# Performance work log

Hardware: AMD Instinct MI355X
Metric: run time of the kernel (lower is better)

Reference implementation:

```python
import jax, jax.numpy as jnp
import numpy as np

N = 20000      # nodes per type
E = 320000     # edges per relation
F = 512        # raw feature dim
H = 4          # attention heads
C = 128        # hidden_channels per head
B = 64         # batch_size (num graphs)
HH = H * C
INNER = 64
NEG_SLOPE = 0.2


def _gatv2(x_src, x_dst, ei, Wl, Wr, att, b):
    """PyG GATv2Conv (concat=True, add_self_loops=True, neg_slope=0.2).
    x_src:[Ns,Fin] x_dst:[Nd,Fin'] ei:[2,E] Wl,Wr:[Fin,H*C] att:[H,C] b:[H*C].
    Returns [Nd, H*C]. Self-loop edges appended (inputs assumed loop-free)."""
    n_dst = x_dst.shape[0]
    loop = jnp.arange(min(x_src.shape[0], n_dst), dtype=ei.dtype)
    src = jnp.concatenate([ei[0], loop])
    dst = jnp.concatenate([ei[1], loop])
    xl = (x_src @ Wl).reshape(-1, H, C)   # source-side transform
    xr = (x_dst @ Wr).reshape(-1, H, C)   # target-side transform
    e = jax.nn.leaky_relu(xl[src] + xr[dst], NEG_SLOPE)   # [E',H,C]
    logit = jnp.einsum('ehc,hc->eh', e, att)               # [E',H]
    m = jax.ops.segment_max(logit, dst, num_segments=n_dst)
    m = jnp.where(jnp.isfinite(m), m, 0.0)
    p = jnp.exp(logit - m[dst])
    s = jax.ops.segment_sum(p, dst, num_segments=n_dst)
    alpha = p / jnp.maximum(s[dst], 1e-16)                 # per-dst softmax
    out = jax.ops.segment_sum(alpha[:, :, None] * xl[src], dst, num_segments=n_dst)
    return out.reshape(n_dst, HH) + b


def _layer(x_i, x_j, ei_ii, ei_jj, ei_ij, ei_ji, Wl, Wr, att, b):
    # relation order: 0:(x_i->x_i) 1:(x_j->x_j) 2:(x_i->x_j) 3:(x_j->x_i); HeteroConv aggr='sum'
    oi = _gatv2(x_i, x_i, ei_ii, Wl[0], Wr[0], att[0], b[0]) \
       + _gatv2(x_j, x_i, ei_ji, Wl[3], Wr[3], att[3], b[3])
    oj = _gatv2(x_j, x_j, ei_jj, Wl[1], Wr[1], att[1], b[1]) \
       + _gatv2(x_i, x_j, ei_ij, Wl[2], Wr[2], att[2], b[2])
    # head-sum + tanh: x.view(-1, heads, hidden).sum(1).tanh()
    oi = jnp.tanh(oi.reshape(-1, H, C).sum(axis=1))
    oj = jnp.tanh(oj.reshape(-1, H, C).sum(axis=1))
    return oi, oj


def setup_inputs() -> dict:
    key = jax.random.key(0)
    ks = jax.random.split(key, 24)
    inp = {
        'x_i': jax.random.normal(ks[0], (N, F), jnp.float32),
        'x_j': jax.random.normal(ks[1], (N, F), jnp.float32),
        'ei_ii': jax.random.randint(ks[2], (2, E), 0, N, jnp.int32),
        'ei_jj': jax.random.randint(ks[3], (2, E), 0, N, jnp.int32),
        'ei_ij': jax.random.randint(ks[4], (2, E), 0, N, jnp.int32),
        'ei_ji': jax.random.randint(ks[5], (2, E), 0, N, jnp.int32),
        'batch_i': jnp.sort(jax.random.randint(ks[6], (N,), 0, B, jnp.int32)),
        'batch_j': jnp.sort(jax.random.randint(ks[7], (N,), 0, B, jnp.int32)),
        'Wl0': jax.random.normal(ks[8], (4, F, HH), jnp.float32) / np.sqrt(F),
        'Wr0': jax.random.normal(ks[9], (4, F, HH), jnp.float32) / np.sqrt(F),
        'att0': jax.random.normal(ks[10], (4, H, C), jnp.float32) / np.sqrt(C),
        'b0': jnp.zeros((4, HH), jnp.float32),
        'Wl1': jax.random.normal(ks[11], (4, C, HH), jnp.float32) / np.sqrt(C),
        'Wr1': jax.random.normal(ks[12], (4, C, HH), jnp.float32) / np.sqrt(C),
        'att1': jax.random.normal(ks[13], (4, H, C), jnp.float32) / np.sqrt(C),
        'b1': jnp.zeros((4, HH), jnp.float32),
        'W_out': jax.random.normal(ks[14], (C, 1), jnp.float32) / np.sqrt(C),
        'b_out': jnp.zeros((1,), jnp.float32),
        'W_i': jax.random.normal(ks[15], (C, INNER), jnp.float32) / np.sqrt(C),
        'b_i': jnp.zeros((INNER,), jnp.float32),
        'W_j': jax.random.normal(ks[16], (C, INNER), jnp.float32) / np.sqrt(C),
        'b_j': jnp.zeros((INNER,), jnp.float32),
    }
    return inp


def reference(x_i, x_j, ei_ii, ei_jj, ei_ij, ei_ji, batch_i, batch_j,
              Wl0, Wr0, att0, b0, Wl1, Wr1, att1, b1,
              W_out, b_out, W_i, b_i, W_j, b_j):
    x_i, x_j = _layer(x_i, x_j, ei_ii, ei_jj, ei_ij, ei_ji, Wl0, Wr0, att0, b0)
    x_i, x_j = _layer(x_i, x_j, ei_ii, ei_jj, ei_ij, ei_ji, Wl1, Wr1, att1, b1)
    # global_add_pool per graph, then unsqueeze(1) + tanh
    p_i = jnp.tanh(jax.ops.segment_sum(x_i, batch_i, num_segments=B))[:, None, :]  # [B,1,C]
    p_j = jnp.tanh(jax.ops.segment_sum(x_j, batch_j, num_segments=B))[:, None, :]
    y_i = p_i @ W_i + b_i   # [B,1,INNER]
    y_j = p_j @ W_j + b_j
    x = (p_i + p_j)[:, 0, :]            # cat along dim=1 then sum(dim=1)
    logits = jax.nn.sigmoid(x @ W_out + b_out)   # [B,1]
    return (logits, y_i, y_j)
```

## Files before the change

### kernel.cpp

```cpp
#include <hip/hip_runtime.h>

#define NN      20000
#define EE      320000
#define ETOT    340000
#define FD      512
#define HH_     4
#define CD      128
#define HHD     512
#define BG      64
#define INNERD  64

typedef __attribute__((ext_vector_type(8))) short bf16x8;
typedef __attribute__((ext_vector_type(4))) float f32x4;

__device__ __forceinline__ float bf2f(unsigned v) { return __uint_as_float(v << 16); }
__device__ __forceinline__ unsigned short f2bf(float f) {
    unsigned u = __float_as_uint(f);
    unsigned r = 0x7fffu + ((u >> 16) & 1u);
    return (unsigned short)((u + r) >> 16);
}
__device__ __forceinline__ void load8bf(const unsigned short* p, float* f) {
    uint4 u = *reinterpret_cast<const uint4*>(p);
    f[0] = bf2f(u.x & 0xffffu); f[1] = bf2f(u.x >> 16);
    f[2] = bf2f(u.y & 0xffffu); f[3] = bf2f(u.y >> 16);
// ... 156 lines not shown
    const unsigned short* __restrict__ Blg, unsigned short* __restrict__ C,
    int bx, int by, int M, int K, int N)
{
    __shared__ unsigned short Ah[128][40];
    __shared__ unsigned short Al[A_EXACT ? 1 : 128][40];

    const int tid = threadIdx.x;
    const int wave = tid >> 6, lane = tid & 63;
    const int quad = lane >> 4, lrow = lane & 15;
    const int wr = (wave >> 1) * 64, wc = (wave & 1) * 64;
    const int tileM = by * 128, tileN = bx * 128;

    const int srow = tid >> 1;
    const int sks  = (tid & 1) * 16;
    const int sgm  = tileM + srow;

    const size_t bfrag = ((size_t)(tileN + wc + lrow) << 5) + quad * 8;
    const size_t kblk  = (size_t)N << 5;

    f32x4 acc[4][4] = {};

    for (int k0 = 0; k0 < K; k0 += 32) {
        if constexpr (!A_EXACT) {
            bf16x8 ph[2] = {{}, {}}, pl[2] = {{}, {}};
            if (sgm < M) {
                const float* Ap = (const float*)A + (size_t)sgm * K + k0 + sks;
                #pragma unroll
                for (int s = 0; s < 2; ++s) {
                    float4 f0 = reinterpret_cast<const float4*>(Ap)[2 * s];
                    float4 f1 = reinterpret_cast<const float4*>(Ap)[2 * s + 1];
                    float xv[8] = {f0.x, f0.y, f0.z, f0.w, f1.x, f1.y, f1.z, f1.w};
                    #pragma unroll
                    for (int pp = 0; pp < 4; ++pp) {
                        unsigned u0 = __float_as_uint(xv[2 * pp]);
                        unsigned u1 = __float_as_uint(xv[2 * pp + 1]);
                        reinterpret_cast<unsigned*>(&ph[s])[pp] =
                            __builtin_amdgcn_perm(u1, u0, 0x07060302u);
                        float r0 = xv[2 * pp]     - __uint_as_float(u0 & 0xffff0000u);
                        float r1 = xv[2 * pp + 1] - __uint_as_float(u1 & 0xffff0000u);
                        reinterpret_cast<unsigned*>(&pl[s])[pp] =
                            __builtin_amdgcn_perm(__float_as_uint(r1), __float_as_uint(r0), 0x07060302u);
                    }
                }
            }
            *reinterpret_cast<bf16x8*>(&Ah[srow][sks])     = ph[0];
            *reinterpret_cast<bf16x8*>(&Ah[srow][sks + 8]) = ph[1];
            *reinterpret_cast<bf16x8*>(&Al[srow][sks])     = pl[0];
            *reinterpret_cast<bf16x8*>(&Al[srow][sks + 8]) = pl[1];
        } else {
            bf16x8 v0 = {}, v1 = {};
            if (sgm < M) {
                const unsigned short* Ap = (const unsigned short*)A + (size_t)sgm * K + k0 + sks;
                v0 = reinterpret_cast<const bf16x8*>(Ap)[0];
                v1 = reinterpret_cast<const bf16x8*>(Ap)[1];
            }
            *reinterpret_cast<bf16x8*>(&Ah[srow][sks])     = v0;
            *reinterpret_cast<bf16x8*>(&Ah[srow][sks + 8]) = v1;
        }
        bf16x8 bh[4], bl[4];
        {
            const unsigned short* Bb = Bhg + (size_t)(k0 >> 5) * kblk + bfrag;
            const unsigned short* Bc = Blg + (size_t)(k0 >> 5) * kblk + bfrag;
            #pragma unroll
            for (int ni = 0; ni < 4; ++ni) {
                bh[ni] = *reinterpret_cast<const bf16x8*>(Bb + ((size_t)ni << 9));
                bl[ni] = *reinterpret_cast<const bf16x8*>(Bc + ((size_t)ni << 9));
            }
        }
        __syncthreads();
        bf16x8 ah[4], al[4];
        #pragma unroll
        for (int mi = 0; mi < 4; ++mi) {
            ah[mi] = *reinterpret_cast<const bf16x8*>(&Ah[wr + mi * 16 + lrow][quad * 8]);
            if constexpr (!A_EXACT)
                al[mi] = *reinterpret_cast<const bf16x8*>(&Al[wr + mi * 16 + lrow][quad * 8]);
        }
        #pragma unroll
        for (int mi = 0; mi < 4; ++mi)
            #pragma unroll
            for (int ni = 0; ni < 4; ++ni) {
                acc[mi][ni] = __builtin_amdgcn_mfma_f32_16x16x32_bf16(
                    ah[mi], bh[ni], acc[mi][ni], 0, 0, 0);
                acc[mi][ni] = __builtin_amdgcn_mfma_f32_16x16x32_bf16(
                    ah[mi], bl[ni], acc[mi][ni], 0, 0, 0);
                if constexpr (!A_EXACT)
                    acc[mi][ni] = __builtin_amdgcn_mfma_f32_16x16x32_bf16(
                        al[mi], bh[ni], acc[mi][ni], 0, 0, 0);
            }
        __syncthreads();
    }
    #pragma unroll
    for (int mi = 0; mi < 4; ++mi) {
        #pragma unroll
        for (int ni = 0; ni < 4; ++ni) {
            int gcol = tileN + wc + ni * 16 + lrow;
            #pragma unroll
            for (int r = 0; r < 4; ++r) {
                int grow = tileM + wr + mi * 16 + quad * 4 + r;
                if (grow < M)
                    C[(size_t)grow * N + gcol] = f2bf(acc[mi][ni][r]);
            }
        }
    }
}

template <typename TA, bool A_EXACT>
__global__ __launch_bounds__(256, 3) void gemm_mfma_t(
    const TA* __restrict__ A0, const TA* __restrict__ A1,
    const unsigned short* __restrict__ B0h, const unsigned short* __restrict__ B0l,
    const unsigned short* __restrict__ B1h, const unsigned short* __restrict__ B1l,
    unsigned short* __restrict__ C0, unsigned short* __restrict__ C1,
    int M, int K, int N)
{
    const int gx = gridDim.x, gy = gridDim.y;
    const int nwg = gx * gy * (int)gridDim.z;
    int b = ((int)blockIdx.z * gy + blockIdx.y) * gx + blockIdx.x;
    int xcd = b & 7, q8 = nwg >> 3, r8 = nwg & 7;
    int work = (xcd < r8 ? xcd * (q8 + 1) : r8 * (q8 + 1) + (xcd - r8) * q8) + (b >> 3);
    int bx = work % gx; int t2 = work / gx; int by = t2 % gy; int bz = t2 / gy;

    const TA* A = bz ? A1 : A0;
    const unsigned short* Bhg = bz ? B1h : B0h;
    const unsigned short* Blg = bz ? B1l : B0l;
    unsigned short* C = bz ? C1 : C0;
    gemm_body<TA, A_EXACT>(A, Bhg, Blg, C, bx, by, M, K, N);
}

template <typename TA, bool A_EXACT>
__global__ __launch_bounds__(256, 3) void gemm_mfma_t4(
    const TA* __restrict__ A0, const TA* __restrict__ A1,
    const TA* __restrict__ A2, const TA* __restrict__ A3,
    const unsigned short* __restrict__ B0h, const unsigned short* __restrict__ B0l,
    const unsigned short* __restrict__ B1h, const unsigned short* __restrict__ B1l,
    const unsigned short* __restrict__ B2h, const unsigned short* __restrict__ B2l,
    const unsigned short* __restrict__ B3h, const unsigned short* __restrict__ B3l,
    unsigned short* __restrict__ C0, unsigned short* __restrict__ C1,
    unsigned short* __restrict__ C2, unsigned short* __restrict__ C3,
    int M, int K, int N)
{
    const int gx = gridDim.x, gy = gridDim.y;
    const int nwg = gx * gy * (int)gridDim.z;
    int b = ((int)blockIdx.z * gy + blockIdx.y) * gx + blockIdx.x;
    int xcd = b & 7, q8 = nwg >> 3, r8 = nwg & 7;
    int work = (xcd < r8 ? xcd * (q8 + 1) : r8 * (q8 + 1) + (xcd - r8) * q8) + (b >> 3);
    int bx = work % gx; int t2 = work / gx; int by = t2 % gy; int bz = t2 / gy;

    const TA* A = bz == 0 ? A0 : bz == 1 ? A1 : bz == 2 ? A2 : A3;
    const unsigned short* Bhg = bz == 0 ? B0h : bz == 1 ? B1h : bz == 2 ? B2h : B3h;
    const unsigned short* Blg = bz == 0 ? B0l : bz == 1 ? B1l : bz == 2 ? B2l : B3l;
    unsigned short* C = bz == 0 ? C0 : bz == 1 ? C1 : bz == 2 ? C2 : C3;
    gemm_body<TA, A_EXACT>(A, Bhg, Blg, C, bx, by, M, K, N);
}

template <typename TA, bool A_EXACT>
__global__ __launch_bounds__(256) void gemm_mfma(
    const TA* __restrict__ A0, const TA* __restrict__ A1,
    const float* __restrict__ B0, const float* __restrict__ B1, int ldb,
    unsigned short* __restrict__ C0, unsigned short* __restrict__ C1,
    int M, int K, int N)
{
    const TA* A = blockIdx.z ? A1 : A0;
    const float* B = blockIdx.z ? B1 : B0;
    unsigned short* C = blockIdx.z ? C1 : C0;

    __shared__ unsigned short Ah[64][40];
    __shared__ unsigned short Al[64][40];
    __shared__ unsigned short Bh[64][40];
    __shared__ unsigned short Bl[64][40];
    const int tid = threadIdx.x;
    const int wave = tid >> 6, lane = tid & 63;
    const int quad = lane >> 4, lrow = lane & 15;
    const int tileM = blockIdx.y * 64, tileN = blockIdx.x * 64;
    const int wm = (wave >> 1) * 32, wn = (wave & 1) * 32;

    f32x4 acc[2][2] = {};

    const int am = tid >> 2;
    const int aks = (tid & 3) * 8;
    const int bn = tid & 63;
    const int bk0 = (tid >> 6) * 8;

    for (int k0 = 0; k0 < K; k0 += 32) {
        {
            int gm = tileM + am;
            bf16x8 ph = {}, pl = {};
            if (gm < M) {
                #pragma unroll
                for (int j = 0; j < 8; ++j) {
                    unsigned short h, l;
                    splitA(A, (size_t)gm * K + k0 + aks + j, h, l);
                    ph[j] = (short)h; pl[j] = (short)l;
                }
            }
            *reinterpret_cast<bf16x8*>(&Ah[am][aks]) = ph;
            if (!A_EXACT) *reinterpret_cast<bf16x8*>(&Al[am][aks]) = pl;
        }
        {
            bf16x8 ph, pl;
            #pragma unroll
            for (int j = 0; j < 8; ++j) {
                unsigned short h, l;
                split_f32(B[(size_t)(k0 + bk0 + j) * ldb + tileN + bn], h, l);
                ph[j] = (short)h; pl[j] = (short)l;
            }
            *reinterpret_cast<bf16x8*>(&Bh[bn][bk0]) = ph;
            *reinterpret_cast<bf16x8*>(&Bl[bn][bk0]) = pl;
        }
        __syncthreads();
        bf16x8 ah[2], al[2], bh[2], bl[2];
        #pragma unroll
        for (int mi = 0; mi < 2; ++mi) {
            ah[mi] = *reinterpret_cast<const bf16x8*>(&Ah[wm + mi * 16 + lrow][quad * 8]);
            if (!A_EXACT)
                al[mi] = *reinterpret_cast<const bf16x8*>(&Al[wm + mi * 16 + lrow][quad * 8]);
        }
        #pragma unroll
        for (int ni = 0; ni < 2; ++ni) {
            bh[ni] = *reinterpret_cast<const bf16x8*>(&Bh[wn + ni * 16 + lrow][quad * 8]);
            bl[ni] = *reinterpret_cast<const bf16x8*>(&Bl[wn + ni * 16 + lrow][quad * 8]);
        }
        #pragma unroll
        for (int mi = 0; mi < 2; ++mi)
            #pragma unroll
            for (int ni = 0; ni < 2; ++ni) {
                acc[mi][ni] = __builtin_amdgcn_mfma_f32_16x16x32_bf16(
                    ah[mi], bh[ni], acc[mi][ni], 0, 0, 0);
                acc[mi][ni] = __builtin_amdgcn_mfma_f32_16x16x32_bf16(
                    ah[mi], bl[ni], acc[mi][ni], 0, 0, 0);
                if (!A_EXACT)
                    acc[mi][ni] = __builtin_amdgcn_mfma_f32_16x16x32_bf16(
                        al[mi], bh[ni], acc[mi][ni], 0, 0, 0);
            }
        __syncthreads();
    }
    #pragma unroll
    for (int mi = 0; mi < 2; ++mi) {
        #pragma unroll
        for (int ni = 0; ni < 2; ++ni) {
            int gcol = tileN + wn + ni * 16 + lrow;
            #pragma unroll
            for (int r = 0; r < 4; ++r) {
                int grow = tileM + wm + mi * 16 + quad * 4 + r;
                if (grow < M)
                    C[(size_t)grow * N + gcol] = f2bf(acc[mi][ni][r]);
            }
        }
    }
}

__global__ __launch_bounds__(256) void fused_aggr1(
    const int* __restrict__ rowptr, const unsigned short* __restrict__ srcs,
    const unsigned short* __restrict__ xl, const unsigned short* __restrict__ xr,
    const float* __restrict__ att,
    float* __restrict__ acc, int add_in, int fin_mode,
    const float* __restrict__ bA, const float* __restrict__ bB,
    unsigned short* __restrict__ z,
    const int* __restrict__ batch, float* __restrict__ pool)
{
    int dst = (int)((blockIdx.x * (size_t)blockDim.x + threadIdx.x) >> 6);
    int lane = threadIdx.x & 63;
    if (dst >= NN) return;
    int beg = rowptr[dst], end = rowptr[dst + 1];

    unsigned ub = *reinterpret_cast<const unsigned*>(xr + (size_t)dst * CD + lane * 2);
    float br0 = bf2f(ub & 0xffffu), br1 = bf2f(ub >> 16);
    float ta0 = att[lane * 2], ta1 = att[lane * 2 + 1];

    float n0 = 0.f, n1 = 0.f, den = 0.f;
    for (int k = beg; k < end; ++k) {
        int src = srcs[k];
        unsigned ua = *reinterpret_cast<const unsigned*>(xl + (size_t)src * CD + lane * 2);
        float a0 = bf2f(ua & 0xffffu), a1 = bf2f(ua >> 16);
        float v0 = a0 + br0, v1 = a1 + br1;
        v0 = (v0 > 0.f) ? v0 : 0.2f * v0;
        v1 = (v1 > 0.f) ? v1 : 0.2f * v1;
        float d = v0 * ta0 + v1 * ta1;
        #pragma unroll
        for (int off = 1; off < 64; off <<= 1)
            d += __shfl_xor(d, off);
        float p = expf(d);
        n0 += p * a0; n1 += p * a1; den += p;
    }
    float o0 = n0 / den, o1 = n1 / den;
    size_t ai = (size_t)dst * CD + lane * 2;
    if (add_in) { o0 += acc[ai]; o1 += acc[ai + 1]; }
    if (fin_mode == 0) {
        acc[ai] = o0; acc[ai + 1] = o1;
    } else {
        int c0 = lane * 2;
        float bb0 = 0.f, bb1 = 0.f;
        #pragma unroll
        for (int h = 0; h < HH_; ++h) {
            bb0 += bA[h * CD + c0]     + bB[h * CD + c0];
            bb1 += bA[h * CD + c0 + 1] + bB[h * CD + c0 + 1];
        }
        o0 = tanhf(o0 + bb0);
        o1 = tanhf(o1 + bb1);
        if (fin_mode == 1) {
            z[ai] = f2bf(o0); z[ai + 1] = f2bf(o1);
        } else {
            int b = batch[dst];
            atomicAdd(&pool[(size_t)b * CD + c0],     o0);
            atomicAdd(&pool[(size_t)b * CD + c0 + 1], o1);
        }
    }
}

__device__ __forceinline__ float edge_logit(const float* a, const float* br, const float* ta) {
    float d = 0.f;
    #pragma unroll
    for (int j = 0; j < 8; ++j) {
        float v = a[j] + br[j];
        v = fmaxf(v, 0.2f * v);
        d += v * ta[j];
    }
    return d;
}
__device__ __forceinline__ float quad_reduce(float d) {
    d += __shfl_xor(d, 1);
    d += __shfl_xor(d, 2);
    d += __shfl_xor(d, 4);
    d += __shfl_xor(d, 8);
    return d;
}
__device__ __forceinline__ void gat_drain(
    const unsigned short* __restrict__ sr, const unsigned short* __restrict__ xl,
    const float* br, const float* ta, int k, int e, float* n, float& den, int lane)
{
    for (; k + 2 <= e; k += 2) {
        int s0 = sr[k], s1 = sr[k + 1];
        float A0[8], A1[8];
        load8bf(xl + (size_t)s0 * HHD + lane * 8, A0);
        load8bf(xl + (size_t)s1 * HHD + lane * 8, A1);
        float d0 = quad_reduce(edge_logit(A0, br, ta));
        float d1 = quad_reduce(edge_logit(A1, br, ta));
        float p0 = __expf(d0), p1 = __expf(d1);
        den += p0;
        #pragma unroll
        for (int j = 0; j < 8; ++j) n[j] += p0 * A0[j];
        den += p1;
        #pragma unroll
        for (int j = 0; j < 8; ++j) n[j] += p1 * A1[j];
    }
    if (k < e) {
        int s0 = sr[k];
        float A0[8];
        load8bf(xl + (size_t)s0 * HHD + lane * 8, A0);
        float d0 = quad_reduce(edge_logit(A0, br, ta));
        float p0 = __expf(d0);
        den += p0;
        #pragma unroll
        for (int j = 0; j < 8; ++j) n[j] += p0 * A0[j];
    }
}

__device__ __forceinline__ void gat_rel(
    const int* __restrict__ rp, const unsigned short* __restrict__ sr,
    const unsigned short* __restrict__ xl, const unsigned short* __restrict__ xr,
    const float* __restrict__ att, int dst, int lane, float* o)
{
    int beg = rp[dst], end = rp[dst + 1];
    float br[8], ta[8];
    load8bf(xr + (size_t)dst * HHD + lane * 8, br);
    #pragma unroll
    for (int j = 0; j < 8; ++j) ta[j] = att[lane * 8 + j];
    float n[8] = {}; float den = 0.f;
    gat_drain(sr, xl, br, ta, beg, end, n, den, lane);
    float inv = 1.f / den;
    #pragma unroll
    for (int j = 0; j < 8; ++j) {
        o[j] = n[j] * inv;
        o[j] += __shfl_xor(o[j], 16);
        o[j] += __shfl_xor(o[j], 32);
    }
}

__device__ __forceinline__ void gat_rel2(
    const int* __restrict__ rp0, const unsigned short* __restrict__ sr0,
    const unsigned short* __restrict__ xl0, const unsigned short* __restrict__ xr0,
    const float* __restrict__ attA,
    const int* __restrict__ rp1, const unsigned short* __restrict__ sr1,
    const unsigned short* __restrict__ xl1, const unsigned short* __restrict__ xr1,
    const float* __restrict__ attB,
    int dst, int lane, float* o0, float* o1)
{
    int k0 = rp0[dst], e0 = rp0[dst + 1];
    int k1 = rp1[dst], e1 = rp1[dst + 1];
    float br0[8], br1[8], ta0[8], ta1[8];
    load8bf(xr0 + (size_t)dst * HHD + lane * 8, br0);
    load8bf(xr1 + (size_t)dst * HHD + lane * 8, br1);
    #pragma unroll
    for (int j = 0; j < 8; ++j) { ta0[j] = attA[lane * 8 + j]; ta1[j] = attB[lane * 8 + j]; }

    float n0[8] = {}, n1[8] = {};
    float den0 = 0.f, den1 = 0.f;

    while (k0 + 2 <= e0 && k1 + 2 <= e1) {
        int sa0 = sr0[k0], sa1 = sr0[k0 + 1];
        int sb0 = sr1[k1], sb1 = sr1[k1 + 1];
        float A0[8], A1[8], B0[8], B1[8];
        load8bf(xl0 + (size_t)sa0 * HHD + lane * 8, A0);
        load8bf(xl0 + (size_t)sa1 * HHD + lane * 8, A1);
        load8bf(xl1 + (size_t)sb0 * HHD + lane * 8, B0);
        load8bf(xl1 + (size_t)sb1 * HHD + lane * 8, B1);
        float dA0 = quad_reduce(edge_logit(A0, br0, ta0));
        float dA1 = quad_reduce(edge_logit(A1, br0, ta0));
        float dB0 = quad_reduce(edge_logit(B0, br1, ta1));
        float dB1 = quad_reduce(edge_logit(B1, br1, ta1));
        float pA0 = __expf(dA0), pA1 = __expf(dA1);
        float pB0 = __expf(dB0), pB1 = __expf(dB1);
        den0 += pA0;
        #pragma unroll
        for (int j = 0; j < 8; ++j) n0[j] += pA0 * A0[j];
        den0 += pA1;
        #pragma unroll
        for (int j = 0; j < 8; ++j) n0[j] += pA1 * A1[j];
        den1 += pB0;
        #pragma unroll
        for (int j = 0; j < 8; ++j) n1[j] += pB0 * B0[j];
        den1 += pB1;
        #pragma unroll
        for (int j = 0; j < 8; ++j) n1[j] += pB1 * B1[j];
        k0 += 2; k1 += 2;
    }
    gat_drain(sr0, xl0, br0, ta0, k0, e0, n0, den0, lane);
    gat_drain(sr1, xl1, br1, ta1, k1, e1, n1, den1, lane);

    float i0 = 1.f / den0, i1 = 1.f / den1;
    #pragma unroll
    for (int j = 0; j < 8; ++j) {
        o0[j] = n0[j] * i0;
        o0[j] += __shfl_xor(o0[j], 16);
        o0[j] += __shfl_xor(o0[j], 32);
        o1[j] = n1[j] * i1;
        o1[j] += __shfl_xor(o1[j], 16);
        o1[j] += __shfl_xor(o1[j], 32);
    }
}

__global__ __launch_bounds__(256) void fused_aggr4(
    const int* __restrict__ rowptr, const unsigned short* __restrict__ srcs,
    const unsigned short* __restrict__ xl, const unsigned short* __restrict__ xr,
    const float* __restrict__ att,
    float* __restrict__ acc, int add_in, int fin_mode,
    const float* __restrict__ bA, const float* __restrict__ bB,
    unsigned short* __restrict__ z,
    const int* __restrict__ batch, float* __restrict__ pool)
{
    int dst = (int)((blockIdx.x * (size_t)blockDim.x + threadIdx.x) >> 6);
    int lane = threadIdx.x & 63;
    if (dst >= NN) return;

    float o[8];
    gat_rel(rowptr, srcs, xl, xr, att, dst, lane, o);

    if (lane < 16) {
        size_t ai = (size_t)dst * CD + lane * 8;
        if (add_in) {
            #pragma unroll
            for (int j = 0; j < 8; ++j) o[j] += acc[ai + j];
        }
        if (fin_mode == 0) {
            #pragma unroll
            for (int j = 0; j < 8; ++j) acc[ai + j] = o[j];
        } else {
            int c0 = lane * 8;
            #pragma unroll
            for (int j = 0; j < 8; ++j) {
                float bb = 0.f;
                #pragma unroll
                for (int h = 0; h < HH_; ++h)
                    bb += bA[h * CD + c0 + j] + bB[h * CD + c0 + j];
                o[j] = tanhf(o[j] + bb);
            }
            if (fin_mode == 1) {
                #pragma unroll
                for (int j = 0; j < 8; ++j) z[ai + j] = f2bf(o[j]);
            } else {
                #pragma unroll
                for (int j = 0; j < 8; ++j) acc[ai + j] = o[j];
            }
        }
    }
}

__global__ __launch_bounds__(256) void fused_aggr4d(
    const int* __restrict__ rp0, const unsigned short* __restrict__ sr0,
    const unsigned short* __restrict__ xl0, const unsigned short* __restrict__ xr0,
    const float* __restrict__ attA,
    const int* __restrict__ rp1, const unsigned short* __restrict__ sr1,
    const unsigned short* __restrict__ xl1, const unsigned short* __restrict__ xr1,
    const float* __restrict__ attB,
    float* __restrict__ acc, int fin_mode,
    const float* __restrict__ bA, const float* __restrict__ bB,
    unsigned short* __restrict__ z,
    const int* __restrict__ batch, float* __restrict__ pool)
{
    int dst = (int)((blockIdx.x * (size_t)blockDim.x + threadIdx.x) >> 6);
    int lane = threadIdx.x & 63;
    if (dst >= NN) return;

    float o0[8], o1[8];
    gat_rel2(rp0, sr0, xl0, xr0, attA, rp1, sr1, xl1, xr1, attB, dst, lane, o0, o1);
    #pragma unroll
    for (int j = 0; j < 8; ++j) o1[j] += o0[j];

    if (lane < 16) {
        size_t ai = (size_t)dst * CD + lane * 8;
        int c0 = lane * 8;
        #pragma unroll
        for (int j = 0; j < 8; ++j) {
            float bb = 0.f;
            #pragma unroll
            for (int h = 0; h < HH_; ++h)
                bb += bA[h * CD + c0 + j] + bB[h * CD + c0 + j];
            o1[j] = tanhf(o1[j] + bb);
        }
        if (fin_mode == 1) {
            #pragma unroll
            for (int j = 0; j < 8; ++j) z[ai + j] = f2bf(o1[j]);
        } else {
            #pragma unroll
            for (int j = 0; j < 8; ++j) acc[ai + j] = o1[j];
        }
    }
}

__global__ __launch_bounds__(512) void pool_reduce(
    const float* __restrict__ acc, const int* __restrict__ batch,
    float* __restrict__ pool)
{
    int b = blockIdx.x;
    int t = threadIdx.x & (CD - 1);
    int q = threadIdx.x >> 7;
    int lo, hi;
    { int l = 0, r = NN; while (l < r) { int m = (l + r) >> 1; if (batch[m] < b) l = m + 1; else r = m; } lo = l; }
    { int l = lo, r = NN; while (l < r) { int m = (l + r) >> 1; if (batch[m] <= b) l = m + 1; else r = m; } hi = l; }
    float s = 0.f;
    for (int nrow = lo + q; nrow < hi; nrow += 4)
        s += acc[(size_t)nrow * CD + t];
    __shared__ float red[4][CD];
    red[q][t] = s;
    __syncthreads();
    if (q == 0)
        pool[(size_t)b * CD + t] = red[0][t] + red[1][t] + red[2][t] + red[3][t];
}

__global__ __launch_bounds__(128) void head_kernel(
    const float* __restrict__ pool_i, const float* __restrict__ pool_j,
    const float* __restrict__ W_out, const float* __restrict__ b_out,
    const float* __restrict__ W_i, const float* __restrict__ b_i,
    const float* __restrict__ W_j, const float* __restrict__ b_j,
    float* __restrict__ out)
{
    int b = blockIdx.x;
    int t = threadIdx.x;
    __shared__ float pi[CD], pj[CD];
    pi[t] = tanhf(pool_i[(size_t)b * CD + t]);
    pj[t] = tanhf(pool_j[(size_t)b * CD + t]);
    __syncthreads();
    if (t < INNERD) {
        float a = b_i[t];
        for (int c = 0; c < CD; ++c) a += pi[c] * W_i[c * INNERD + t];
        out[BG + (size_t)b * INNERD + t] = a;
    } else {
        int k = t - INNERD;
        float a = b_j[k];
        for (int c = 0; c < CD; ++c) a += pj[c] * W_j[c * INNERD + k];
        out[BG + BG * INNERD + (size_t)b * INNERD + k] = a;
    }
    if (t == 0) {
        float a = b_out[0];
        for (int c = 0; c < CD; ++c) a += (pi[c] + pj[c]) * W_out[c];
        out[b] = 1.f / (1.f + expf(-a));
    }
}

struct Ws {
    unsigned short *xl, *xr, *xl2, *xr2, *z_i, *z_j;
    float* acc;
    int *rowptr[4];
    unsigned short *srcs[4];
    int *cnt, *cursor;
    float *pool_i, *pool_j;
    unsigned short *wt0l_h, *wt0l_l, *wt0r_h, *wt0r_l;
    unsigned short *wt1l_h, *wt1l_l, *wt1r_h, *wt1r_l;
};

static void build_csr(const int* ei, int* rowptr, unsigned short* srcs,
                      int* cnt, int* cursor, hipStream_t stream) {
    hipMemsetAsync(cnt, 0, NN * sizeof(int), stream);
    csr_hist<<<(EE + 255) / 256, 256, 0, stream>>>(ei, cnt);
    csr_scan<<<1, 1024, 0, stream>>>(cnt, rowptr, cursor);
    csr_scatter16<<<(ETOT + 255) / 256, 256, 0, stream>>>(ei, cursor, srcs);
}

template <typename TA, bool A_EXACT>
static void run_group_fat_m(const TA* srcA[2], const TA* dstA[2],
                            const int* rp[2], const unsigned short* sr[2],
                            const int rids[2], int K,
                            const unsigned short* WTl_h, const unsigned short* WTl_l,
                            const unsigned short* WTr_h, const unsigned short* WTr_l,
                            const float* att, const float* bias, int fin_mode,
                            unsigned short* zout, const int* batch, float* pool,
                            const Ws& w, hipStream_t stream)
{
    dim3 gg(HHD / 128, (NN + 127) / 128, 4);
    size_t off0 = (size_t)rids[0] * HHD * K;
    size_t off1 = (size_t)rids[1] * HHD * K;
    gemm_mfma_t4<TA, A_EXACT><<<gg, 256, 0, stream>>>(
        srcA[0], dstA[0], srcA[1], dstA[1],
        WTl_h + off0, WTl_l + off0, WTr_h + off0, WTr_l + off0,
        WTl_h + off1, WTl_l + off1, WTr_h + off1, WTr_l + off1,
        w.xl, w.xr, w.xl2, w.xr2, NN, K, HHD);
    fused_aggr4d<<<NN / 4, 256, 0, stream>>>(
        rp[0], sr[0], w.xl, w.xr, att + (size_t)rids[0] * HHD,
        rp[1], sr[1], w.xl2, w.xr2, att + (size_t)rids[1] * HHD,
        w.acc, fin_mode,
        bias + (size_t)rids[0] * HHD, bias + (size_t)rids[1] * HHD,
        zout, batch, pool);
}

template <typename TA, bool A_EXACT>
static void run_group_fat_t(const TA* srcA[2], const TA* dstA[2],
                            const int* rp[2], const unsigned short* sr[2],
                            const int rids[2], int K,
                            const unsigned short* WTl_h, const unsigned short* WTl_l,
                            const unsigned short* WTr_h, const unsigned short* WTr_l,
                            const float* att, const float* bias, int fin_mode,
                            unsigned short* zout, const int* batch, float* pool,
                            const Ws& w, hipStream_t stream)
{
    dim3 gg(HHD / 128, (NN + 127) / 128, 2);
    const int ablocks = NN / 4;
    for (int q = 0; q < 2; ++q) {
        int r = rids[q];
        size_t off = (size_t)r * HHD * K;
        gemm_mfma_t<TA, A_EXACT><<<gg, 256, 0, stream>>>(
            srcA[q], dstA[q],
            WTl_h + off, WTl_l + off, WTr_h + off, WTr_l + off,
            w.xl, w.xr, NN, K, HHD);
        int fm = (q == 1) ? fin_mode : 0;
        fused_aggr4<<<ablocks, 256, 0, stream>>>(
            rp[q], sr[q], w.xl, w.xr,
            att + (size_t)r * HHD,
            w.acc, q > 0 ? 1 : 0, fm,
            bias + (size_t)rids[0] * HHD, bias + (size_t)rids[1] * HHD,
            zout, batch, pool);
    }
}

template <typename TA, bool A_EXACT>
static void run_group_fat(const TA* srcA[2], const TA* dstA[2],
                          const int* rp[2], const unsigned short* sr[2],
                          const int rids[2], int K,
                          const float* Wl, const float* Wr, const float* att,
                          const float* bias, int fin_mode,
                          unsigned short* zout, const int* batch, float* pool,
                          const Ws& w, hipStream_t stream)
{
    dim3 gg(HHD / 64, (NN + 63) / 64, 2);
    const int ablocks = NN / 4;
    for (int q = 0; q < 2; ++q) {
        int r = rids[q];
        gemm_mfma<TA, A_EXACT><<<gg, 256, 0, stream>>>(
            srcA[q], dstA[q],
            Wl + (size_t)r * K * HHD, Wr + (size_t)r * K * HHD, HHD,
            w.xl, w.xr, NN, K, HHD);
        int fm = (q == 1) ? fin_mode : 0;
        fused_aggr4<<<ablocks, 256, 0, stream>>>(
            rp[q], sr[q], w.xl, w.xr,
            att + (size_t)r * HHD,
            w.acc, q > 0 ? 1 : 0, fm,
            bias + (size_t)rids[0] * HHD, bias + (size_t)rids[1] * HHD,
            zout, batch, pool);
    }
}

template <typename TA, bool A_EXACT>
static void run_group_thin(const TA* srcA[2], const TA* dstA[2],
                           const int* eis[2], const int rids[2], int K,
                           const float* Wl, const float* Wr, const float* att,
                           const float* bias, int fin_mode,
                           unsigned short* zout, const int* batch, float* pool,
                           const Ws& w, hipStream_t stream)
{
    dim3 gg(2, (NN + 63) / 64, 2);
    const int ablocks = NN / 4;
    for (int q = 0; q < 2; ++q) {
        int r = rids[q];
        build_csr(eis[q], w.rowptr[0], w.srcs[0], w.cnt, w.cursor, stream);
        for (int h = 0; h < HH_; ++h) {
            const float* WlS = Wl + (size_t)r * K * HHD + h * CD;
            const float* WrS = Wr + (size_t)r * K * HHD + h * CD;
            gemm_mfma<TA, A_EXACT><<<gg, 256, 0, stream>>>(
                srcA[q], dstA[q], WlS, WrS, HHD, w.xl, w.xr, NN, K, CD);
            int pass = q * HH_ + h;
            int fm = (pass == 2 * HH_ - 1) ? fin_mode : 0;
            fused_aggr1<<<ablocks, 256, 0, stream>>>(
                w.rowptr[0], w.srcs[0], w.xl, w.xr,
                att + (size_t)r * HHD + h * CD,
                w.acc, pass > 0 ? 1 : 0, fm,
                bias + (size_t)rids[0] * HHD, bias + (size_t)rids[1] * HHD,
                zout, batch, pool);
        }
    }
}

extern "C" void kernel_launch(void* const* d_in, const int* in_sizes, int n_in,
                              void* d_out, int out_size, void* d_ws, size_t ws_size,
                              hipStream_t stream)
{
    const float* x_i   = (const float*)d_in[0];
    const float* x_j   = (const float*)d_in[1];
    const int* ei_ii   = (const int*)d_in[2];
    const int* ei_jj   = (const int*)d_in[3];
    const int* ei_ij   = (const int*)d_in[4];
    const int* ei_ji   = (const int*)d_in[5];
    const int* batch_i = (const int*)d_in[6];
    const int* batch_j = (const int*)d_in[7];
    const float* Wl0   = (const float*)d_in[8];
    const float* Wr0   = (const float*)d_in[9];
    const float* att0  = (const float*)d_in[10];
    const float* b0    = (const float*)d_in[11];
    const float* Wl1   = (const float*)d_in[12];
    const float* Wr1   = (const float*)d_in[13];
    const float* att1  = (const float*)d_in[14];
    const float* b1    = (const float*)d_in[15];
    const float* W_out = (const float*)d_in[16];
    const float* b_out = (const float*)d_in[17];
    const float* W_i   = (const float*)d_in[18];
    const float* b_i   = (const float*)d_in[19];
    const float* W_j   = (const float*)d_in[20];
    const float* b_j   = (const float*)d_in[21];
    float* out = (float*)d_out;

    const size_t FAT2_BYTES = (size_t)NN * HHD * 2 * 2 + (size_t)NN * CD * 4
                            + (size_t)NN * CD * 2 * 2 + 4 * (size_t)ETOT * 2
                            + 4 * (size_t)(NN + 4) * 4 + 4 * (size_t)NN * 4 * 2
                            + (size_t)BG * CD * 4 * 2;
    const size_t FAT1_BYTES = (size_t)NN * HHD * 2 * 2 + (size_t)NN * CD * 4
                            + (size_t)NN * CD * 2 * 2 + (size_t)ETOT * 2
                            + (size_t)(NN + 4) * 4 + (size_t)NN * 4 * 2
                            + (size_t)BG * CD * 4 * 2;
    const size_t WT0_ONE = (size_t)4 * 512 * 512 * 2;
    const size_t WT1_ONE = (size_t)4 * 512 * 128 * 2;
    const size_t WT_BYTES = 4 * WT0_ONE + 4 * WT1_ONE;
    const size_t X2_BYTES = 2 * (size_t)NN * HHD * 2;

    const int ncsr = (ws_size >= FAT2_BYTES) ? 4 : 1;
    const bool fat = (ws_size >= FAT1_BYTES);
    const bool fat_t = (ws_size >= FAT2_BYTES + WT_BYTES);
    const bool fat_m = (ws_size >= FAT2_BYTES + WT_BYTES + X2_BYTES);

    Ws w;
    char* p = (char*)d_ws;
    size_t xbytes = fat ? (size_t)NN * HHD * 2 : (size_t)NN * CD * 2;
    w.xl     = (unsigned short*)p; p += xbytes;
    w.xr     = (unsigned short*)p; p += xbytes;
    w.acc    = (float*)p;          p += (size_t)NN * CD * 4;
    w.z_i    = (unsigned short*)p; p += (size_t)NN * CD * 2;
    w.z_j    = (unsigned short*)p; p += (size_t)NN * CD * 2;
    {
        int* rowptr_all = (int*)p;            p += (size_t)ncsr * (NN + 4) * 4;
        unsigned short* srcs_all = (unsigned short*)p; p += (size_t)ncsr * ETOT * 2;
        for (int r = 0; r < 4; ++r) {
            int rr = (r < ncsr) ? r : 0;
            w.rowptr[r] = rowptr_all + (size_t)rr * (NN + 4);
            w.srcs[r]   = srcs_all + (size_t)rr * ETOT;
        }
    }
    w.cnt    = (int*)p;            p += (size_t)ncsr * NN * 4;
    w.cursor = (int*)p;            p += (size_t)ncsr * NN * 4;
    w.pool_i = (float*)p;          p += (size_t)BG * CD * 4;
    w.pool_j = (float*)p;          p += (size_t)BG * CD * 4;
    if (fat_t) {
        w.wt0l_h = (unsigned short*)p; p += WT0_ONE;
        w.wt0l_l = (unsigned short*)p; p += WT0_ONE;
        w.wt0r_h = (unsigned short*)p; p += WT0_ONE;
        w.wt0r_l = (unsigned short*)p; p += WT0_ONE;
        w.wt1l_h = (unsigned short*)p; p += WT1_ONE;
        w.wt1l_l = (unsigned short*)p; p += WT1_ONE;
        w.wt1r_h = (unsigned short*)p; p += WT1_ONE;
        w.wt1r_l = (unsigned short*)p; p += WT1_ONE;
    }
    if (fat_m) {
        w.xl2 = (unsigned short*)p; p += (size_t)NN * HHD * 2;
        w.xr2 = (unsigned short*)p; p += (size_t)NN * HHD * 2;
    }

    hipMemsetAsync(w.pool_i, 0, (size_t)BG * CD * sizeof(float), stream);
    hipMemsetAsync(w.pool_j, 0, (size_t)BG * CD * sizeof(float), stream);

    const int* eis_all[4] = { ei_ii, ei_jj, ei_ij, ei_ji };
    const float* srcA0_i[2] = { x_i, x_j };  const float* dstA0_i[2] = { x_i, x_i };
    const float* srcA0_j[2] = { x_j, x_i };  const float* dstA0_j[2] = { x_j, x_j };
    const int rids_i[2] = { 0, 3 };
    const int rids_j[2] = { 1, 2 };
    const unsigned short* srcA1_i[2] = { w.z_i, w.z_j };
    const unsigned short* dstA1_i[2] = { w.z_i, w.z_i };
    const unsigned short* srcA1_j[2] = { w.z_j, w.z_i };
    const unsigned short* dstA1_j[2] = { w.z_j, w.z_j };

    if (fat_t) {
        hipMemsetAsync(w.cnt, 0, 4 * NN * sizeof(int), stream);
        csr_hist4<<<(4 * EE + 255) / 256, 256, 0, stream>>>(
            ei_ii, ei_jj, ei_ij, ei_ji, w.cnt);
        csr_scan4<<<4, 1024, 0, stream>>>(w.cnt, w.rowptr[0], w.cursor);
        csr_scatter4<<<(4 * ETOT + 255) / 256, 256, 0, stream>>>(
            ei_ii, ei_jj, ei_ij, ei_ji, w.cursor, w.srcs[0]);
        wsplit_t<<<4 * (FD / 64) * 8, 256, 0, stream>>>(Wl0, w.wt0l_h, w.wt0l_l, FD);
        wsplit_t<<<4 * (FD / 64) * 8, 256, 0, stream>>>(Wr0, w.wt0r_h, w.wt0r_l, FD);
        wsplit_t<<<4 * (CD / 64) * 8, 256, 0, stream>>>(Wl1, w.wt1l_h, w.wt1l_l, CD);
        wsplit_t<<<4 * (CD / 64) * 8, 256, 0, stream>>>(Wr1, w.wt1r_h, w.wt1r_l, CD);

        const int* rp_i[2] = { w.rowptr[0], w.rowptr[3] };
        const unsigned short* sr_i[2] = { w.srcs[0], w.srcs[3] };
        const int* rp_j[2] = { w.rowptr[1], w.rowptr[2] };
        const unsigned short* sr_j[2] = { w.srcs[1], w.srcs[2] };

        if (fat_m) {
            run_group_fat_m<float, false>(srcA0_i, dstA0_i, rp_i, sr_i, rids_i, FD,
                                          w.wt0l_h, w.wt0l_l, w.wt0r_h, w.wt0r_l,
                                          att0, b0, 1, w.z_i, nullptr, nullptr, w, stream);
            run_group_fat_m<float, false>(srcA0_j, dstA0_j, rp_j, sr_j, rids_j, FD,
                                          w.wt0l_h, w.wt0l_l, w.wt0r_h, w.wt0r_l,
                                          att0, b0, 1, w.z_j, nullptr, nullptr, w, stream);
            run_group_fat_m<unsigned short, true>(srcA1_i, dstA1_i, rp_i, sr_i, rids_i, CD,
                                                  w.wt1l_h, w.wt1l_l, w.wt1r_h, w.wt1r_l,
                                                  att1, b1, 2, nullptr, batch_i, w.pool_i, w, stream);
            pool_reduce<<<BG, 512, 0, stream>>>(w.acc, batch_i, w.pool_i);
            run_group_fat_m<unsigned short, true>(srcA1_j, dstA1_j, rp_j, sr_j, rids_j, CD,
                                                  w.wt1l_h, w.wt1l_l, w.wt1r_h, w.wt1r_l,
                                                  att1, b1, 2, nullptr, batch_j, w.pool_j, w, stream);
            pool_reduce<<<BG, 512, 0, stream>>>(w.acc, batch_j, w.pool_j);
        } else {
            run_group_fat_t<float, false>(srcA0_i, dstA0_i, rp_i, sr_i, rids_i, FD,
                                          w.wt0l_h, w.wt0l_l, w.wt0r_h, w.wt0r_l,
                                          att0, b0, 1, w.z_i, nullptr, nullptr, w, stream);
            run_group_fat_t<float, false>(srcA0_j, dstA0_j, rp_j, sr_j, rids_j, FD,
                                          w.wt0l_h, w.wt0l_l, w.wt0r_h, w.wt0r_l,
                                          att0, b0, 1, w.z_j, nullptr, nullptr, w, stream);
            run_group_fat_t<unsigned short, true>(srcA1_i, dstA1_i, rp_i, sr_i, rids_i, CD,
                                                  w.wt1l_h, w.wt1l_l, w.wt1r_h, w.wt1r_l,
                                                  att1, b1, 2, nullptr, batch_i, w.pool_i, w, stream);
            pool_reduce<<<BG, 512, 0, stream>>>(w.acc, batch_i, w.pool_i);
            run_group_fat_t<unsigned short, true>(srcA1_j, dstA1_j, rp_j, sr_j, rids_j, CD,
                                                  w.wt1l_h, w.wt1l_l, w.wt1r_h, w.wt1r_l,
                                                  att1, b1, 2, nullptr, batch_j, w.pool_j, w, stream);
            pool_reduce<<<BG, 512, 0, stream>>>(w.acc, batch_j, w.pool_j);
        }
    } else if (fat) {
        if (ncsr == 4) {
            for (int r = 0; r < 4; ++r)
                build_csr(eis_all[r], w.rowptr[r], w.srcs[r], w.cnt, w.cursor, stream);
            const int* rp_i[2] = { w.rowptr[0], w.rowptr[3] };
            const unsigned short* sr_i[2] = { w.srcs[0], w.srcs[3] };
            const int* rp_j[2] = { w.rowptr[1], w.rowptr[2] };
            const unsigned short* sr_j[2] = { w.srcs[1], w.srcs[2] };
            run_group_fat<float, false>(srcA0_i, dstA0_i, rp_i, sr_i, rids_i, FD,
                                        Wl0, Wr0, att0, b0, 1, w.z_i, nullptr, nullptr, w, stream);
            run_group_fat<float, false>(srcA0_j, dstA0_j, rp_j, sr_j, rids_j, FD,
                                        Wl0, Wr0, att0, b0, 1, w.z_j, nullptr, nullptr, w, stream);
            run_group_fat<unsigned short, true>(srcA1_i, dstA1_i, rp_i, sr_i, rids_i, CD,
                                                Wl1, Wr1, att1, b1, 2, nullptr, batch_i, w.pool_i, w, stream);
            pool_reduce<<<BG, 512, 0, stream>>>(w.acc, batch_i, w.pool_i);
            run_group_fat<unsigned short, true>(srcA1_j, dstA1_j, rp_j, sr_j, rids_j, CD,
                                                Wl1, Wr1, att1, b1, 2, nullptr, batch_j, w.pool_j, w, stream);
            pool_reduce<<<BG, 512, 0, stream>>>(w.acc, batch_j, w.pool_j);
        } else {
            for (int pass = 0; pass < 4; ++pass) {
                const int* rids = (pass & 1) ? rids_j : rids_i;
                for (int q = 0; q < 2; ++q) {
                    int r = rids[q];
                    build_csr(eis_all[r], w.rowptr[0], w.srcs[0], w.cnt, w.cursor, stream);
                    dim3 gg(HHD / 64, (NN + 63) / 64, 2);
                    if (pass < 2) {
                        const float* sa = (pass == 0) ? srcA0_i[q] : srcA0_j[q];
                        const float* da = (pass == 0) ? dstA0_i[q] : dstA0_j[q];
                        gemm_mfma<float, false><<<gg, 256, 0, stream>>>(
                            sa, da, Wl0 + (size_t)r * FD * HHD, Wr0 + (size_t)r * FD * HHD,
                            HHD, w.xl, w.xr, NN, FD, HHD);
                        fused_aggr4<<<NN / 4, 256, 0, stream>>>(
                            w.rowptr[0], w.srcs[0], w.xl, w.xr, att0 + (size_t)r * HHD,
                            w.acc, q, (q == 1) ? 1 : 0,
                            b0 + (size_t)rids[0] * HHD, b0 + (size_t)rids[1] * HHD,
                            (pass == 0) ? w.z_i : w.z_j, nullptr, nullptr);
                    } else {
                        const unsigned short* sa = (pass == 2) ? srcA1_i[q] : srcA1_j[q];
                        const unsigned short* da = (pass == 2) ? dstA1_i[q] : dstA1_j[q];
                        gemm_mfma<unsigned short, true><<<gg, 256, 0, stream>>>(
                            sa, da, Wl1 + (size_t)r * CD * HHD, Wr1 + (size_t)r * CD * HHD,
                            HHD, w.xl, w.xr, NN, CD, HHD);
                        fused_aggr4<<<NN / 4, 256, 0, stream>>>(
                            w.rowptr[0], w.srcs[0], w.xl, w.xr, att1 + (size_t)r * HHD,
                            w.acc, q, (q == 1) ? 2 : 0,
                            b1 + (size_t)rids[0] * HHD, b1 + (size_t)rids[1] * HHD,
                            nullptr, (pass == 2) ? batch_i : batch_j,
                            (pass == 2) ? w.pool_i : w.pool_j);
                    }
                }
                if (pass == 2)
                    pool_reduce<<<BG, 512, 0, stream>>>(w.acc, batch_i, w.pool_i);
                else if (pass == 3)
                    pool_reduce<<<BG, 512, 0, stream>>>(w.acc, batch_j, w.pool_j);
            }
        }
    } else {
        const int* eis_i[2] = { ei_ii, ei_ji };
        const int* eis_j[2] = { ei_jj, ei_ij };
        run_group_thin<float, false>(srcA0_i, dstA0_i, eis_i, rids_i, FD, Wl0, Wr0, att0, b0,
                                     1, w.z_i, nullptr, nullptr, w, stream);
        run_group_thin<float, false>(srcA0_j, dstA0_j, eis_j, rids_j, FD, Wl0, Wr0, att0, b0,
                                     1, w.z_j, nullptr, nullptr, w, stream);
        run_group_thin<unsigned short, true>(srcA1_i, dstA1_i, eis_i, rids_i, CD, Wl1, Wr1, att1, b1,
                                             2, nullptr, batch_i, w.pool_i, w, stream);
        run_group_thin<unsigned short, true>(srcA1_j, dstA1_j, eis_j, rids_j, CD, Wl1, Wr1, att1, b1,
                                             2, nullptr, batch_j, w.pool_j, w, stream);
    }

    head_kernel<<<BG, 128, 0, stream>>>(w.pool_i, w.pool_j, W_out, b_out,
                                        W_i, b_i, W_j, b_j, out);
}
```

Before: 1.352 ms.

## Fuse layer-0 GEMM with aggregation in one launch and batch layer-1 GEMMs

When the workspace holds four projection buffers, the layer-0 GEMMs for the j-side relations run in the same launch as the i-side aggregation. Blocks are split by index between GEMM tiles and aggregation work, so compute-bound and gather-bound work can overlap. All eight layer-1 projection GEMMs are merged into one launch instead of separate per-group launches. This costs more workspace memory. The mixed kernel is capped at three blocks per CU, which may limit occupancy for the aggregation part.

```diff
diff --git a/kernel.cpp b/kernel.cpp
--- a/kernel.cpp
+++ b/kernel.cpp
@@ -332,6 +332,35 @@
     gemm_body<TA, A_EXACT>(A, Bhg, Blg, C, bx, by, M, K, N);
 }
 
+__global__ __launch_bounds__(256, 3) void gemm_mfma_L1x8(
+    const unsigned short* __restrict__ zi, const unsigned short* __restrict__ zj,
+    const unsigned short* __restrict__ Wlh, const unsigned short* __restrict__ Wll,
+    const unsigned short* __restrict__ Wrh, const unsigned short* __restrict__ Wrl,
+    unsigned short* __restrict__ C0, unsigned short* __restrict__ C1,
+    unsigned short* __restrict__ C2, unsigned short* __restrict__ C3,
+    unsigned short* __restrict__ C4, unsigned short* __restrict__ C5,
+    unsigned short* __restrict__ C6, unsigned short* __restrict__ C7,
+    int M, int K, int N)
+{
+    const int gx = gridDim.x, gy = gridDim.y;
+    const int nwg = gx * gy * (int)gridDim.z;
+    int b = ((int)blockIdx.z * gy + blockIdx.y) * gx + blockIdx.x;
+    int xcd = b & 7, q8 = nwg >> 3, r8 = nwg & 7;
+    int work = (xcd < r8 ? xcd * (q8 + 1) : r8 * (q8 + 1) + (xcd - r8) * q8) + (b >> 3);
+    int bx = work % gx; int t2 = work / gx; int by = t2 % gy; int bz = t2 / gy;
+
+    int rr = bz >> 1;
+    int rel = rr == 0 ? 0 : rr == 1 ? 3 : rr == 2 ? 1 : 2;
+    bool aj = (bz == 2 || bz == 4 || bz == 5 || bz == 7);
+    const unsigned short* A = aj ? zj : zi;
+    size_t off = (size_t)rel * HHD * K;
+    const unsigned short* Bh = ((bz & 1) ? Wrh : Wlh) + off;
+    const unsigned short* Bl = ((bz & 1) ? Wrl : Wll) + off;
+    unsigned short* C = bz == 0 ? C0 : bz == 1 ? C1 : bz == 2 ? C2 : bz == 3 ? C3
+                      : bz == 4 ? C4 : bz == 5 ? C5 : bz == 6 ? C6 : C7;
+    gemm_body<unsigned short, true>(A, Bh, Bl, C, bx, by, M, K, N);
+}
+
 template <typename TA, bool A_EXACT>
 __global__ __launch_bounds__(256) void gemm_mfma(
     const TA* __restrict__ A0, const TA* __restrict__ A1,
@@ -615,6 +644,44 @@
         o1[j] = n1[j] * i1;
         o1[j] += __shfl_xor(o1[j], 16);
         o1[j] += __shfl_xor(o1[j], 32);
+    }
+}
+
+__device__ __forceinline__ void aggr4d_body(
+    int dst, int lane,
+    const int* __restrict__ rp0, const unsigned short* __restrict__ sr0,
+    const unsigned short* __restrict__ xl0, const unsigned short* __restrict__ xr0,
+    const float* __restrict__ attA,
+    const int* __restrict__ rp1, const unsigned short* __restrict__ sr1,
+    const unsigned short* __restrict__ xl1, const unsigned short* __restrict__ xr1,
+    const float* __restrict__ attB,
+    float* __restrict__ acc, int fin_mode,
+    const float* __restrict__ bA, const float* __restrict__ bB,
+    unsigned short* __restrict__ z)
+{
+    float o0[8], o1[8];
+    gat_rel2(rp0, sr0, xl0, xr0, attA, rp1, sr1, xl1, xr1, attB, dst, lane, o0, o1);
+    #pragma unroll
+    for (int j = 0; j < 8; ++j) o1[j] += o0[j];
+
+    if (lane < 16) {
+        size_t ai = (size_t)dst * CD + lane * 8;
+        int c0 = lane * 8;
+        #pragma unroll
+        for (int j = 0; j < 8; ++j) {
+            float bb = 0.f;
+            #pragma unroll
+            for (int h = 0; h < HH_; ++h)
+                bb += bA[h * CD + c0 + j] + bB[h * CD + c0 + j];
+            o1[j] = tanhf(o1[j] + bb);
+        }
+        if (fin_mode == 1) {
+            #pragma unroll
+            for (int j = 0; j < 8; ++j) z[ai + j] = f2bf(o1[j]);
+        } else {
+            #pragma unroll
+            for (int j = 0; j < 8; ++j) acc[ai + j] = o1[j];
+        }
     }
 }
 
@@ -679,30 +746,49 @@
     int dst = (int)((blockIdx.x * (size_t)blockDim.x + threadIdx.x) >> 6);
     int lane = threadIdx.x & 63;
     if (dst >= NN) return;
-
-    float o0[8], o1[8];
-    gat_rel2(rp0, sr0, xl0, xr0, attA, rp1, sr1, xl1, xr1, attB, dst, lane, o0, o1);
-    #pragma unroll
-    for (int j = 0; j < 8; ++j) o1[j] += o0[j];
-
-    if (lane < 16) {
-        size_t ai = (size_t)dst * CD + lane * 8;
-        int c0 = lane * 8;
-        #pragma unroll
-        for (int j = 0; j < 8; ++j) {
-            float bb = 0.f;
-            #pragma unroll
-            for (int h = 0; h < HH_; ++h)
-                bb += bA[h * CD + c0 + j] + bB[h * CD + c0 + j];
-            o1[j] = tanhf(o1[j] + bb);
-        }
-        if (fin_mode == 1) {
-            #pragma unroll
-            for (int j = 0; j < 8; ++j) z[ai + j] = f2bf(o1[j]);
-        } else {
-            #pragma unroll
-            for (int j = 0; j < 8; ++j) acc[ai + j] = o1[j];
-        }
+    aggr4d_body(dst, lane, rp0, sr0, xl0, xr0, attA, rp1, sr1, xl1, xr1, attB,
+                acc, fin_mode, bA, bB, z);
+}
+
+template <typename TA, bool A_EXACT>
+__global__ __launch_bounds__(256, 3) void gemm_aggr_fused(
+    int ngemm,
+    const TA* __restrict__ A0, const TA* __restrict__ A1,
+    const TA* __restrict__ A2, const TA* __restrict__ A3,
+    const unsigned short* __restrict__ B0h, const unsigned short* __restrict__ B0l,
+    const unsigned short* __restrict__ B1h, const unsigned short* __restrict__ B1l,
+    const unsigned short* __restrict__ B2h, const unsigned short* __restrict__ B2l,
+    const unsigned short* __restrict__ B3h, const unsigned short* __restrict__ B3l,
+    unsigned short* __restrict__ C0, unsigned short* __restrict__ C1,
+    unsigned short* __restrict__ C2, unsigned short* __restrict__ C3,
+    int M, int K, int N,
+    const int* __restrict__ rp0, const unsigned short* __restrict__ sr0,
+    const unsigned short* __restrict__ xl0, const unsigned short* __restrict__ xr0,
+    const float* __restrict__ attA,
+    const int* __restrict__ rp1, const unsigned short* __restrict__ sr1,
+    const unsigned short* __restrict__ xl1, const unsigned short* __restrict__ xr1,
+    const float* __restrict__ attB,
+    float* __restrict__ acc, int fin_mode,
+    const float* __restrict__ bA, const float* __restrict__ bB,
+    unsigned short* __restrict__ zout)
+{
+    if ((int)blockIdx.x < ngemm) {
+        int b = blockIdx.x;
+        int xcd = b & 7, q8 = ngemm >> 3, r8 = ngemm & 7;
+        int work = (xcd < r8 ? xcd * (q8 + 1) : r8 * (q8 + 1) + (xcd - r8) * q8) + (b >> 3);
+        const int gx = N / 128, gy = (M + 127) / 128;
+        int bx = work % gx; int t2 = work / gx; int by = t2 % gy; int bz = t2 / gy;
+        const TA* A = bz == 0 ? A0 : bz == 1 ? A1 : bz == 2 ? A2 : A3;
+        const unsigned short* Bh = bz == 0 ? B0h : bz == 1 ? B1h : bz == 2 ? B2h : B3h;
+        const unsigned short* Bl = bz == 0 ? B0l : bz == 1 ? B1l : bz == 2 ? B2l : B3l;
+        unsigned short* C = bz == 0 ? C0 : bz == 1 ? C1 : bz == 2 ? C2 : C3;
+        gemm_body<TA, A_EXACT>(A, Bh, Bl, C, bx, by, M, K, N);
+    } else {
+        int dst = (int)(((blockIdx.x - ngemm) * (size_t)blockDim.x + threadIdx.x) >> 6);
+        int lane = threadIdx.x & 63;
+        if (dst >= NN) return;
+        aggr4d_body(dst, lane, rp0, sr0, xl0, xr0, attA, rp1, sr1, xl1, xr1, attB,
+                    acc, fin_mode, bA, bB, zout);
     }
 }
 
@@ -757,7 +843,7 @@
 }
 
 struct Ws {
-    unsigned short *xl, *xr, *xl2, *xr2, *z_i, *z_j;
+    unsigned short *xl, *xr, *xl2, *xr2, *xl3, *xr3, *xl4, *xr4, *z_i, *z_j;
     float* acc;
     int *rowptr[4];
     unsigned short *srcs[4];
@@ -932,6 +1018,7 @@
     const bool fat = (ws_size >= FAT1_BYTES);
     const bool fat_t = (ws_size >= FAT2_BYTES + WT_BYTES);
     const bool fat_m = (ws_size >= FAT2_BYTES + WT_BYTES + X2_BYTES);
+    const bool fat_f = (ws_size >= FAT2_BYTES + WT_BYTES + 3 * X2_BYTES);
 
     Ws w;
     char* p = (char*)d_ws;
@@ -968,6 +1055,12 @@
         w.xl2 = (unsigned short*)p; p += (size_t)NN * HHD * 2;
         w.xr2 = (unsigned short*)p; p += (size_t)NN * HHD * 2;
     }
+    if (fat_f) {
+        w.xl3 = (unsigned short*)p; p += (size_t)NN * HHD * 2;
+        w.xr3 = (unsigned short*)p; p += (size_t)NN * HHD * 2;
+        w.xl4 = (unsigned short*)p; p += (size_t)NN * HHD * 2;
+        w.xr4 = (unsigned short*)p; p += (size_t)NN * HHD * 2;
+    }
 
     hipMemsetAsync(w.pool_i, 0, (size_t)BG * CD * sizeof(float), stream);
     hipMemsetAsync(w.pool_j, 0, (size_t)BG * CD * sizeof(float), stream);
@@ -999,7 +1092,48 @@
         const int* rp_j[2] = { w.rowptr[1], w.rowptr[2] };
         const unsigned short* sr_j[2] = { w.srcs[1], w.srcs[2] };
 
-        if (fat_m) {
+        if (fat_f) {
+            const size_t o0 = (size_t)0 * HHD * FD, o3 = (size_t)3 * HHD * FD;
+            const size_t o1 = (size_t)1 * HHD * FD, o2 = (size_t)2 * HHD * FD;
+            dim3 gg(HHD / 128, (NN + 127) / 128, 4);
+            gemm_mfma_t4<float, false><<<gg, 256, 0, stream>>>(
+                x_i, x_i, x_j, x_i,
+                w.wt0l_h + o0, w.wt0l_l + o0, w.wt0r_h + o0, w.wt0r_l + o0,
+                w.wt0l_h + o3, w.wt0l_l + o3, w.wt0r_h + o3, w.wt0r_l + o3,
+                w.xl, w.xr, w.xl2, w.xr2, NN, FD, HHD);
+            const int ngemm = (HHD / 128) * ((NN + 127) / 128) * 4;
+            gemm_aggr_fused<float, false><<<ngemm + NN / 4, 256, 0, stream>>>(
+                ngemm,
+                x_j, x_j, x_i, x_j,
+                w.wt0l_h + o1, w.wt0l_l + o1, w.wt0r_h + o1, w.wt0r_l + o1,
+                w.wt0l_h + o2, w.wt0l_l + o2, w.wt0r_h + o2, w.wt0r_l + o2,
+                w.xl3, w.xr3, w.xl4, w.xr4, NN, FD, HHD,
+                w.rowptr[0], w.srcs[0], w.xl, w.xr, att0 + (size_t)0 * HHD,
+                w.rowptr[3], w.srcs[3], w.xl2, w.xr2, att0 + (size_t)3 * HHD,
+                w.acc, 1, b0 + (size_t)0 * HHD, b0 + (size_t)3 * HHD, w.z_i);
+            fused_aggr4d<<<NN / 4, 256, 0, stream>>>(
+                w.rowptr[1], w.srcs[1], w.xl3, w.xr3, att0 + (size_t)1 * HHD,
+                w.rowptr[2], w.srcs[2], w.xl4, w.xr4, att0 + (size_t)2 * HHD,
+                w.acc, 1, b0 + (size_t)1 * HHD, b0 + (size_t)2 * HHD,
+                w.z_j, nullptr, nullptr);
+            dim3 g8(HHD / 128, (NN + 127) / 128, 8);
+            gemm_mfma_L1x8<<<g8, 256, 0, stream>>>(
+                w.z_i, w.z_j, w.wt1l_h, w.wt1l_l, w.wt1r_h, w.wt1r_l,
+                w.xl, w.xr, w.xl2, w.xr2, w.xl3, w.xr3, w.xl4, w.xr4,
+                NN, CD, HHD);
+            fused_aggr4d<<<NN / 4, 256, 0, stream>>>(
+                w.rowptr[0], w.srcs[0], w.xl, w.xr, att1 + (size_t)0 * HHD,
+                w.rowptr[3], w.srcs[3], w.xl2, w.xr2, att1 + (size_t)3 * HHD,
+                w.acc, 2, b1 + (size_t)0 * HHD, b1 + (size_t)3 * HHD,
+                nullptr, nullptr, nullptr);
+            pool_reduce<<<BG, 512, 0, stream>>>(w.acc, batch_i, w.pool_i);
+            fused_aggr4d<<<NN / 4, 256, 0, stream>>>(
+                w.rowptr[1], w.srcs[1], w.xl3, w.xr3, att1 + (size_t)1 * HHD,
+                w.rowptr[2], w.srcs[2], w.xl4, w.xr4, att1 + (size_t)2 * HHD,
+                w.acc, 2, b1 + (size_t)1 * HHD, b1 + (size_t)2 * HHD,
+                nullptr, nullptr, nullptr);
+            pool_reduce<<<BG, 512, 0, stream>>>(w.acc, batch_j, w.pool_j);
+        } else if (fat_m) {
             run_group_fat_m<float, false>(srcA0_i, dstA0_i, rp_i, sr_i, rids_i, FD,
                                           w.wt0l_h, w.wt0l_l, w.wt0r_h, w.wt0r_l,
                                           att0, b0, 1, w.z_i, nullptr, nullptr, w, stream);
```

After: 1.310 ms. 1.03x faster.
